# Kernel tuning notes

Measured on AMD Instinct MI355X. Metric: run time of the kernel, lower is better.

Reference implementation:

```python
import jax, jax.numpy as jnp
import numpy as np

B, SQ, SK, H, NH = 2, 2048, 2048, 2048, 16
HD = H // NH  # 128
NEG = -1e9


def setup_inputs() -> dict:
    key = jax.random.key(0)
    ks = jax.random.split(key, 8)
    hidden_states = jax.random.normal(ks[0], (B, SQ, H), dtype=jnp.float32)
    # key already transposed/expanded for baddbmm: [B*nh, head_dim, key_len]
    k = jax.random.normal(ks[1], (B * NH, HD, SK), dtype=jnp.float32)
    v = jax.random.normal(ks[2], (B, NH, SK, HD), dtype=jnp.float32)
    # additive float causal mask [B, 1, Sq, Sk]
    causal = jnp.tril(jnp.ones((SQ, SK), dtype=bool))
    attention_mask = jnp.where(causal, 0.0, NEG).astype(jnp.float32)
    attention_mask = jnp.broadcast_to(attention_mask[None, None], (B, 1, SQ, SK))
    w_q = jax.random.normal(ks[3], (H, H), dtype=jnp.float32) * 0.02
    b_q = jnp.zeros((H,), dtype=jnp.float32)
    w_proj = jax.random.normal(ks[4], (H, H), dtype=jnp.float32) * 0.02
    b_proj = jnp.zeros((H,), dtype=jnp.float32)
    return {
        "hidden_states": hidden_states,
        "key": k,
        "value": v,
        "attention_mask": attention_mask,
        "w_q": w_q,
        "b_q": b_q,
        "w_proj": w_proj,
        "b_proj": b_proj,
    }


def reference(hidden_states, key, value, attention_mask, w_q, b_q, w_proj, b_proj):
    dtype = hidden_states.dtype
    scale = 1.0 / (HD ** 0.5)  # scale_attn_weights=True, attention_multiplier=None
    # q projection: [B, Sq, H] -> [B, nh, Sq, hd]
    q = hidden_states @ w_q.T + b_q
    q = q.reshape(B, SQ, NH, HD).transpose(0, 2, 1, 3)
    # key comes in as [B*nh, hd, Sk]
    k = key.reshape(B, NH, HD, SK)
    # scores = mask + scale * q @ k  (baddbmm with beta=1)
    scores = attention_mask + scale * jnp.einsum("bhqd,bhdk->bhqk", q, k)
    # softmax in fp32 (attention_softmax_in_fp32=True), cast back
    probs = jax.nn.softmax(scores.astype(jnp.float32), axis=-1).astype(dtype)
    # attn_pdrop=0 -> no dropout
    out = jnp.einsum("bhqk,bhkd->bhqd", probs, value)  # [B, nh, Sq, hd]
    out = out.transpose(0, 2, 1, 3).reshape(B, SQ, H)
    out = out @ w_proj.T + b_proj  # resid_pdrop=0 -> no dropout
    return out
```

## Files before the change

### kernel.cpp

```cpp
#include <hip/hip_runtime.h>
#include <hip/hip_bf16.h>

typedef __bf16 bf16;
typedef __bf16 bf16x4 __attribute__((ext_vector_type(4)));
typedef __bf16 bf16x8 __attribute__((ext_vector_type(8)));
typedef float  f32x4  __attribute__((ext_vector_type(4)));
typedef float  f32x16 __attribute__((ext_vector_type(16)));
typedef unsigned int u32;

#define B_   2
#define SQ_  2048
#define SK_  2048
#define H_   2048
#define NH_  16
#define HD_  128
#define BH_  (B_*NH_)

__device__ inline void gl_lds16(const bf16* g, bf16* l) {
  __builtin_amdgcn_global_load_lds(
      (const __attribute__((address_space(1))) u32*)(const void*)g,
      (__attribute__((address_space(3))) u32*)(void*)l,
      16, 0, 0);
}

__device__ inline float exp2_fast(float x) {
  float r; asm("v_exp_f32 %0, %1" : "=v"(r) : "v"(x)); return r;
}

union PW { u32 w[4]; bf16x8 v; };

__global__ __launch_bounds__(256) void cvt3_f32_bf16(const float* __restrict__ a, bf16* __restrict__ ao,
                                                     const float* __restrict__ b, bf16* __restrict__ bo,
                                                     const float* __restrict__ c, bf16* __restrict__ co) {
  const int blk = blockIdx.x;
  const float* in; bf16* out; int n4, bstart, nblk;
  if (blk < 1024)      { in = a; out = ao; n4 = (B_ * SQ_ * H_) / 4; bstart = 0;    nblk = 1024; }
  else if (blk < 1536) { in = b; out = bo; n4 = (H_ * H_) / 4;       bstart = 1024; nblk = 512; }
  else                 { in = c; out = co; n4 = (H_ * H_) / 4;       bstart = 1536; nblk = 512; }
  int i = (blk - bstart) * 256 + threadIdx.x;
  const int stride = nblk * 256;
  for (; i < n4; i += stride) {
    float4 v = ((const float4*)in)[i];
    bf16x4 w; w[0] = (bf16)v.x; w[1] = (bf16)v.y; w[2] = (bf16)v.z; w[3] = (bf16)v.w;
    ((bf16x4*)out)[i] = w;
  }
}

__global__ __launch_bounds__(256) void transpose_cvt2(const float* __restrict__ key,
                                                      const float* __restrict__ value,
                                                      bf16* __restrict__ kout,
                                                      bf16* __restrict__ vout) {
  __shared__ float tile[64][65];
  const int id = blockIdx.x;
  const float* src; bf16* dst; int R, C, r0, c0, bh;
  if (id < 2048) {
    src = key; dst = kout; R = HD_; C = SK_;
    c0 = (id & 31) * 64; r0 = ((id >> 5) & 1) * 64; bh = id >> 6;
  } else {
    const int j = id - 2048;
    src = value; dst = vout; R = SK_; C = HD_;
    c0 = (j & 1) * 64; r0 = ((j >> 1) & 31) * 64; bh = j >> 6;
  }
  src += (size_t)bh * R * C;
  dst += (size_t)bh * R * C;
  const int t = threadIdx.x;
  const int tx = t & 15, ty = t >> 4;
#pragma unroll
  for (int p = 0; p < 4; ++p) {
    int rr = ty + p * 16;
    float4 v = *(const float4*)&src[(size_t)(r0 + rr) * C + c0 + tx * 4];
    tile[rr][tx * 4 + 0] = v.x; tile[rr][tx * 4 + 1] = v.y;
    tile[rr][tx * 4 + 2] = v.z; tile[rr][tx * 4 + 3] = v.w;
  }
  __syncthreads();
#pragma unroll
  for (int p = 0; p < 4; ++p) {
    int cc = ty + p * 16;
    bf16x4 w;
#pragma unroll
    for (int i = 0; i < 4; ++i) w[i] = (bf16)tile[tx * 4 + i][cc];
    *(bf16x4*)&dst[(size_t)(c0 + cc) * R + r0 + tx * 4] = w;
  }
}

template <typename OutT>
__global__ __launch_bounds__(256) void gemm_bt(const bf16* __restrict__ A,
                                               const bf16* __restrict__ Bw,
                                               const float* __restrict__ bias,
                                               OutT* __restrict__ C,
                                               int M, int N, int K, float osc) {
  __shared__ bf16 Abuf[128 * 32];
  __shared__ bf16 Bbuf[128 * 32];
  const int nbn = N >> 7;
  int wg = blockIdx.x, nwg = gridDim.x;
  int swz = (nwg & 7) ? wg : ((wg & 7) * (nwg >> 3) + (wg >> 3));
  int bm = swz / nbn, bn = swz % nbn;
  const int t = threadIdx.x, lane = t & 63, wid = t >> 6;
  const int r = lane & 15, g = lane >> 4;
  const int wr = wid >> 1, wc = wid & 1;
  const size_t m0 = (size_t)bm * 128, n0 = (size_t)bn * 128;

  f32x4 acc[4][4];
#pragma unroll
  for (int m = 0; m < 4; ++m)
#pragma unroll
    for (int n = 0; n < 4; ++n) acc[m][n] = (f32x4){0.f, 0.f, 0.f, 0.f};

  for (int k0 = 0; k0 < K; k0 += 32) {
    __syncthreads();
#pragma unroll
    for (int p = 0; p < 2; ++p) {
      int c = p * 256 + t;
      int row = c >> 2, off = c & 3;
      gl_lds16(A + (m0 + row) * K + k0 + off * 8, &Abuf[(p * 256 + wid * 64) * 8]);
      gl_lds16(Bw + (n0 + row) * K + k0 + off * 8, &Bbuf[(p * 256 + wid * 64) * 8]);
    }
    __syncthreads();
    bf16x8 af[4], bfr[4];
#pragma unroll
    for (int m = 0; m < 4; ++m)
      af[m] = *(const bf16x8*)&Abuf[(wr * 64 + m * 16 + r) * 32 + g * 8];
#pragma unroll
    for (int n = 0; n < 4; ++n)
      bfr[n] = *(const bf16x8*)&Bbuf[(wc * 64 + n * 16 + r) * 32 + g * 8];
#pragma unroll
    for (int m = 0; m < 4; ++m)
#pragma unroll
      for (int n = 0; n < 4; ++n)
        acc[m][n] = __builtin_amdgcn_mfma_f32_16x16x32_bf16(af[m], bfr[n], acc[m][n], 0, 0, 0);
  }

  float bv[4];
#pragma unroll
  for (int n = 0; n < 4; ++n) bv[n] = bias[n0 + wc * 64 + n * 16 + r];
#pragma unroll
  for (int m = 0; m < 4; ++m)
#pragma unroll
    for (int n = 0; n < 4; ++n)
#pragma unroll
      for (int rr = 0; rr < 4; ++rr) {
        size_t row = m0 + wr * 64 + m * 16 + g * 4 + rr;
        size_t col = n0 + wc * 64 + n * 16 + r;
        C[row * N + col] = (OutT)((acc[m][n][rr] + bv[n]) * osc);
      }
}

__global__ __launch_bounds__(256, 2) void flash_attn(const bf16* __restrict__ Q,
                                                     const bf16* __restrict__ Kt,
                                                     const bf16* __restrict__ Vt,
                                                     bf16* __restrict__ O,
                                                     bf16* __restrict__ part,
                                                     float2* __restrict__ mlbuf) {
  __shared__ bf16 Klds[2][64 * 128];
  __shared__ bf16 Vlds[2][64 * 128];

  const int id = blockIdx.x;
  const int pr = (id >> 3) & 7;
  const int hf = (id >> 6) & 1;
  const int bh = (id & 7) + 8 * (id >> 7);
  const int qtA = 15 - pr, qtB = pr;
  const int nA = 2 * qtA + 2, nB = 2 * qtB + 2;
  const int b = bh >> 4, h = bh & 15;
  const int t = threadIdx.x, lane = t & 63, wid = t >> 6;
  const int l5 = lane & 31, hiL = lane >> 5;

  const bf16* Kbase = Kt + (size_t)bh * SK_ * HD_;
  const bf16* Vbase = Vt + (size_t)bh * HD_ * SK_;

  u32 kSrc[4], vSrc[4];
#pragma unroll
  for (int p = 0; p < 4; ++p) {
    int c = p * 256 + t;
    { int row = c >> 4, off = c & 15, src = off ^ (row & 15);
      kSrc[p] = (u32)(row * HD_ + src * 8); }
    { int srow = c >> 4, j = c & 15, gj = j ^ (srow & 15);
      int d = srow * 2 + (gj >> 3);
      vSrc[p] = (u32)(d * SK_ + (gj & 7) * 8); }
  }

  int cur = 0;
  const int npass = hf ? 2 : 1;
#pragma unroll 1
  for (int ps = 0; ps < npass; ++ps) {
    int qt, lo, hi, partial;
    if (!hf)          { qt = qtA; lo = 0;  hi = 17; partial = 1; }
    else if (ps == 0) { qt = qtA; lo = 17; hi = nA; partial = 1; }
    else              { qt = qtB; lo = 0;  hi = nB; partial = 0; }
    const int qbw = qt * 128 + wid * 32;
    const int q_lane = qbw + l5;

    bf16x8 qf[8];
    {
      const size_t qrow = (size_t)(b * SQ_ + q_lane) * H_ + (size_t)h * HD_;
#pragma unroll
      for (int dt = 0; dt < 8; ++dt)
        qf[dt] = *(const bf16x8*)&Q[qrow + dt * 16 + 8 * hiL];
    }

    f32x16 acc[4];
#pragma unroll
    for (int n = 0; n < 4; ++n)
#pragma unroll
      for (int e = 0; e < 16; ++e) acc[n][e] = 0.f;
    float mrun = -3.0e38f, lpart = 0.f;

    {
      const size_t ks = (size_t)lo * (64 * HD_), vs = (size_t)lo * 64;
#pragma unroll
      for (int p = 0; p < 4; ++p) {
        gl_lds16(Kbase + ks + kSrc[p], &Klds[cur][(p * 256 + wid * 64) * 8]);
        gl_lds16(Vbase + vs + vSrc[p], &Vlds[cur][(p * 256 + wid * 64) * 8]);
      }
    }
    asm volatile("s_waitcnt vmcnt(0)" ::: "memory");
    __syncthreads();

#pragma unroll 1
    for (int st = lo; st < hi; ++st) {
      if (st + 1 < hi) {
        const size_t ks = (size_t)(st + 1) * (64 * HD_), vs = (size_t)(st + 1) * 64;
#pragma unroll
        for (int p = 0; p < 4; ++p) {
          gl_lds16(Kbase + ks + kSrc[p], &Klds[cur ^ 1][(p * 256 + wid * 64) * 8]);
          gl_lds16(Vbase + vs + vSrc[p], &Vlds[cur ^ 1][(p * 256 + wid * 64) * 8]);
        }
      }
      const int s0 = st * 64;

      if (s0 <= qbw + 31) {
        f32x16 sv0, sv1;
#pragma unroll
        for (int e = 0; e < 16; ++e) { sv0[e] = 0.f; sv1[e] = 0.f; }
        __builtin_amdgcn_s_setprio(1);
#pragma unroll
        for (int dt = 0; dt < 8; ++dt) {
          const int dch = ((2 * dt + hiL) ^ (l5 & 15)) * 8;
          bf16x8 kf0 = *(const bf16x8*)&Klds[cur][l5 * 128 + dch];
          bf16x8 kf1 = *(const bf16x8*)&Klds[cur][(32 + l5) * 128 + dch];
          sv0 = __builtin_amdgcn_mfma_f32_32x32x16_bf16(kf0, qf[dt], sv0, 0, 0, 0);
          sv1 = __builtin_amdgcn_mfma_f32_32x32x16_bf16(kf1, qf[dt], sv1, 0, 0, 0);
        }
        __builtin_amdgcn_s_setprio(0);

        if (s0 + 63 > qbw) {
#pragma unroll
          for (int r2 = 0; r2 < 16; ++r2) {
            const int kl = (r2 & 3) + 8 * (r2 >> 2) + 4 * hiL;
            if (s0 + kl > q_lane)      sv0[r2] = -3.0e38f;
            if (s0 + 32 + kl > q_lane) sv1[r2] = -3.0e38f;
          }
        }

        float pm = -3.0e38f;
#pragma unroll
        for (int r2 = 0; r2 < 16; ++r2) pm = fmaxf(pm, fmaxf(sv0[r2], sv1[r2]));
        pm = fmaxf(pm, __shfl_xor(pm, 32));
        if (!__all(pm <= mrun + 10.0f ? 1 : 0)) {
          const float mnew = fmaxf(mrun, pm);
          const float corr = exp2_fast(mrun - mnew);
          mrun = mnew; lpart *= corr;
          const int cb = __float_as_int(corr);
#pragma unroll
          for (int r2 = 0; r2 < 16; ++r2) {
            const int q2 = (r2 & 3) + 8 * (r2 >> 2) + 4 * hiL;
            const float cc = __int_as_float(__builtin_amdgcn_ds_bpermute(q2 * 4, cb));
#pragma unroll
            for (int n = 0; n < 4; ++n) acc[n][r2] *= cc;
          }
        }

        float psum = 0.f;
#pragma unroll
        for (int r2 = 0; r2 < 16; ++r2) {
          sv0[r2] = exp2_fast(sv0[r2] - mrun); psum += sv0[r2];
          sv1[r2] = exp2_fast(sv1[r2] - mrun); psum += sv1[r2];
        }
        lpart += psum;

        bf16x8 pa[4];
#pragma unroll
        for (int h2 = 0; h2 < 2; ++h2) {
          u32 pk[8], px[8];
#pragma unroll
          for (int j = 0; j < 8; ++j) {
            union { bf16 hh[2]; u32 u; } tt;
            float plo = h2 ? sv1[2 * j] : sv0[2 * j];
            float phi = h2 ? sv1[2 * j + 1] : sv0[2 * j + 1];
            tt.hh[0] = (bf16)plo; tt.hh[1] = (bf16)phi;
            pk[j] = tt.u;
          }
#pragma unroll
          for (int j = 0; j < 8; ++j) px[j] = (u32)__shfl_xor((int)pk[j], 32);
          PW a0, a1;
          a0.w[0] = hiL ? px[2] : pk[0]; a0.w[1] = hiL ? px[3] : pk[1];
          a0.w[2] = hiL ? pk[2] : px[0]; a0.w[3] = hiL ? pk[3] : px[1];
          a1.w[0] = hiL ? px[6] : pk[4]; a1.w[1] = hiL ? px[7] : pk[5];
          a1.w[2] = hiL ? pk[6] : px[4]; a1.w[3] = hiL ? pk[7] : px[5];
          pa[2 * h2]     = a0.v;
          pa[2 * h2 + 1] = a1.v;
        }

        __builtin_amdgcn_s_setprio(1);
#pragma unroll
        for (int n = 0; n < 4; ++n) {
          const int sr = n * 16 + (l5 >> 1);
#pragma unroll
          for (int kt = 0; kt < 4; ++kt) {
            const int jj = ((((l5 & 1) << 3) | (2 * kt + hiL)) ^ (l5 >> 1));
            bf16x8 vf = *(const bf16x8*)&Vlds[cur][sr * 128 + jj * 8];
            acc[n] = __builtin_amdgcn_mfma_f32_32x32x16_bf16(pa[kt], vf, acc[n], 0, 0, 0);
          }
        }
        __builtin_amdgcn_s_setprio(0);
      }

      asm volatile("s_waitcnt vmcnt(0)" ::: "memory");
      __syncthreads();
      cur ^= 1;
    }

    float ltot = lpart + __shfl_xor(lpart, 32);
    if (partial) {
      const int slot = (hf * 8 + pr) * 32 + bh;
      bf16* pbase = part + (size_t)slot * (128 * 128);
#pragma unroll
      for (int n = 0; n < 4; ++n)
#pragma unroll
        for (int r2 = 0; r2 < 16; ++r2) {
          const int rowt = wid * 32 + (r2 & 3) + 8 * (r2 >> 2) + 4 * hiL;
          pbase[rowt * 128 + n * 32 + l5] = (bf16)acc[n][r2];
        }
      if (lane < 32)
        mlbuf[(size_t)slot * 128 + wid * 32 + lane] = float2{mrun, ltot};
    } else {
      const float inv = 1.0f / ltot;
      const int ib = __float_as_int(inv);
#pragma unroll
      for (int r2 = 0; r2 < 16; ++r2) {
        const int q2 = (r2 & 3) + 8 * (r2 >> 2) + 4 * hiL;
        const float ic = __int_as_float(__builtin_amdgcn_ds_bpermute(q2 * 4, ib));
        const size_t rowg = (size_t)(b * SQ_ + qbw + q2);
#pragma unroll
        for (int n = 0; n < 4; ++n)
          O[rowg * H_ + (size_t)h * HD_ + n * 32 + l5] = (bf16)(acc[n][r2] * ic);
      }
    }
  }
}

__global__ __launch_bounds__(256) void flash_merge(const bf16* __restrict__ part,
                                                   const float2* __restrict__ mlbuf,
                                                   bf16* __restrict__ O) {
  const int gid = blockIdx.x * 256 + threadIdx.x;
  const int idx = gid >> 4;
  const int d8 = (gid & 15) * 8;
  const int row = idx & 127;
  const int bh = (idx >> 7) & 31;
  const int pr = idx >> 12;
  const int qtA = 15 - pr;
  const int b = bh >> 4, h = bh & 15;
  const int slot0 = pr * 32 + bh;
  const int slot1 = (8 + pr) * 32 + bh;
  const float2 ml0 = mlbuf[(size_t)slot0 * 128 + row];
  const float2 ml1 = mlbuf[(size_t)slot1 * 128 + row];
  const float M = fmaxf(ml0.x, ml1.x);
  const float c0 = exp2_fast(ml0.x - M);
  const float c1 = exp2_fast(ml1.x - M);
  const float inv = 1.0f / (c0 * ml0.y + c1 * ml1.y);
  const bf16x8 a0 = *(const bf16x8*)&part[(size_t)slot0 * (128 * 128) + row * 128 + d8];
  const bf16x8 a1 = *(const bf16x8*)&part[(size_t)slot1 * (128 * 128) + row * 128 + d8];
  bf16x8 o;
#pragma unroll
  for (int j = 0; j < 8; ++j)
    o[j] = (bf16)((c0 * (float)a0[j] + c1 * (float)a1[j]) * inv);
  const size_t orow = (size_t)(b * SQ_ + qtA * 128 + row);
  *(bf16x8*)&O[orow * H_ + (size_t)h * HD_ + d8] = o;
}

extern "C" void kernel_launch(void* const* d_in, const int* in_sizes, int n_in,
                              void* d_out, int out_size, void* d_ws, size_t ws_size,
                              hipStream_t stream) {
  const float* hidden = (const float*)d_in[0];
  const float* key    = (const float*)d_in[1];
  const float* value  = (const float*)d_in[2];
  const float* w_q    = (const float*)d_in[4];
  const float* b_q    = (const float*)d_in[5];
  const float* w_proj = (const float*)d_in[6];
  const float* b_proj = (const float*)d_in[7];
  float* out = (float*)d_out;

  const size_t N_HID = (size_t)B_ * SQ_ * H_;
  const size_t N_W   = (size_t)H_ * H_;
  const size_t N_KV  = (size_t)BH_ * SK_ * HD_;
  const float SC2 = 0.08838834764831845f * 1.4426950408889634f;

  bf16* hid_bf  = (bf16*)d_ws;
  bf16* wq_bf   = hid_bf + N_HID;
  bf16* wp_bf   = wq_bf + N_W;
  bf16* k_bf    = wp_bf + N_W;
  bf16* vt_bf   = k_bf + N_KV;
  bf16* q_bf    = vt_bf + N_KV;
  bf16* part_bf = q_bf + N_HID;
  float2* ml_bf = (float2*)(part_bf + (size_t)512 * 128 * 128);
  bf16* attn_bf = hid_bf;

  cvt3_f32_bf16<<<2048, 256, 0, stream>>>(hidden, hid_bf, w_q, wq_bf, w_proj, wp_bf);
  transpose_cvt2<<<4096, 256, 0, stream>>>(key, value, k_bf, vt_bf);

  gemm_bt<bf16><<<(B_ * SQ_ / 128) * (H_ / 128), 256, 0, stream>>>(
      hid_bf, wq_bf, b_q, q_bf, B_ * SQ_, H_, H_, SC2);

  flash_attn<<<512, 256, 0, stream>>>(q_bf, k_bf, vt_bf, attn_bf, part_bf, ml_bf);
  flash_merge<<<2048, 256, 0, stream>>>(part_bf, ml_bf, attn_bf);

  gemm_bt<float><<<(B_ * SQ_ / 128) * (H_ / 128), 256, 0, stream>>>(
      attn_bf, wp_bf, b_proj, out, B_ * SQ_, H_, H_, 1.0f);
}
```

Measured before the change: 211.1 us.

## Defer P·V MFMAs by one tile to overlap with next QK and softmax

The P·V product for tile i is now issued in iteration i+1, right after the QK^T MFMAs for that tile and before its softmax. The aim is to let matrix work overlap the exp/max/shuffle work of softmax within a wave. V gets a third LDS buffer so the previous tile's V stays resident while the next one loads. A final drain step after the loop handles the last pending tile. The cost is a larger LDS footprint (V grows from two to three buffers), more live registers for the held P fragments, and an extra barrier at the start of each pass.

```diff
diff --git a/kernel.cpp b/kernel.cpp
--- a/kernel.cpp
+++ b/kernel.cpp
@@ -152,7 +152,7 @@
                                                      bf16* __restrict__ part,
                                                      float2* __restrict__ mlbuf) {
   __shared__ bf16 Klds[2][64 * 128];
-  __shared__ bf16 Vlds[2][64 * 128];
+  __shared__ bf16 Vlds[3][64 * 128];
 
   const int id = blockIdx.x;
   const int pr = (id >> 3) & 7;
@@ -178,7 +178,6 @@
       vSrc[p] = (u32)(d * SK_ + (gj & 7) * 8); }
   }
 
-  int cur = 0;
   const int npass = hf ? 2 : 1;
 #pragma unroll 1
   for (int ps = 0; ps < npass; ++ps) {
@@ -204,12 +203,17 @@
       for (int e = 0; e < 16; ++e) acc[n][e] = 0.f;
     float mrun = -3.0e38f, lpart = 0.f;
 
+    bf16x8 paP[4];
+    bool have_prev = false;
+    int kc = 0, vp = 2, vc = 0, vn = 1;
+
+    __syncthreads();
     {
       const size_t ks = (size_t)lo * (64 * HD_), vs = (size_t)lo * 64;
 #pragma unroll
       for (int p = 0; p < 4; ++p) {
-        gl_lds16(Kbase + ks + kSrc[p], &Klds[cur][(p * 256 + wid * 64) * 8]);
-        gl_lds16(Vbase + vs + vSrc[p], &Vlds[cur][(p * 256 + wid * 64) * 8]);
+        gl_lds16(Kbase + ks + kSrc[p], &Klds[0][(p * 256 + wid * 64) * 8]);
+        gl_lds16(Vbase + vs + vSrc[p], &Vlds[0][(p * 256 + wid * 64) * 8]);
       }
     }
     asm volatile("s_waitcnt vmcnt(0)" ::: "memory");
@@ -221,27 +225,47 @@
         const size_t ks = (size_t)(st + 1) * (64 * HD_), vs = (size_t)(st + 1) * 64;
 #pragma unroll
         for (int p = 0; p < 4; ++p) {
-          gl_lds16(Kbase + ks + kSrc[p], &Klds[cur ^ 1][(p * 256 + wid * 64) * 8]);
-          gl_lds16(Vbase + vs + vSrc[p], &Vlds[cur ^ 1][(p * 256 + wid * 64) * 8]);
+          gl_lds16(Kbase + ks + kSrc[p], &Klds[kc ^ 1][(p * 256 + wid * 64) * 8]);
+          gl_lds16(Vbase + vs + vSrc[p], &Vlds[vn][(p * 256 + wid * 64) * 8]);
         }
       }
       const int s0 = st * 64;
-
-      if (s0 <= qbw + 31) {
-        f32x16 sv0, sv1;
+      const bool act = (s0 <= qbw + 31);
+
+      f32x16 sv0, sv1;
+      if (act) {
 #pragma unroll
         for (int e = 0; e < 16; ++e) { sv0[e] = 0.f; sv1[e] = 0.f; }
         __builtin_amdgcn_s_setprio(1);
 #pragma unroll
         for (int dt = 0; dt < 8; ++dt) {
           const int dch = ((2 * dt + hiL) ^ (l5 & 15)) * 8;
-          bf16x8 kf0 = *(const bf16x8*)&Klds[cur][l5 * 128 + dch];
-          bf16x8 kf1 = *(const bf16x8*)&Klds[cur][(32 + l5) * 128 + dch];
+          bf16x8 kf0 = *(const bf16x8*)&Klds[kc][l5 * 128 + dch];
+          bf16x8 kf1 = *(const bf16x8*)&Klds[kc][(32 + l5) * 128 + dch];
           sv0 = __builtin_amdgcn_mfma_f32_32x32x16_bf16(kf0, qf[dt], sv0, 0, 0, 0);
           sv1 = __builtin_amdgcn_mfma_f32_32x32x16_bf16(kf1, qf[dt], sv1, 0, 0, 0);
         }
         __builtin_amdgcn_s_setprio(0);
-
+      }
+
+      if (have_prev) {
+        const bf16* vbuf = &Vlds[vp][0];
+        __builtin_amdgcn_s_setprio(1);
+#pragma unroll
+        for (int n = 0; n < 4; ++n) {
+          const int sr = n * 16 + (l5 >> 1);
+#pragma unroll
+          for (int kt = 0; kt < 4; ++kt) {
+            const int jj = ((((l5 & 1) << 3) | (2 * kt + hiL)) ^ (l5 >> 1));
+            bf16x8 vf = *(const bf16x8*)&vbuf[sr * 128 + jj * 8];
+            acc[n] = __builtin_amdgcn_mfma_f32_32x32x16_bf16(paP[kt], vf, acc[n], 0, 0, 0);
+          }
+        }
+        __builtin_amdgcn_s_setprio(0);
+        have_prev = false;
+      }
+
+      if (act) {
         if (s0 + 63 > qbw) {
 #pragma unroll
           for (int r2 = 0; r2 < 16; ++r2) {
@@ -277,7 +301,6 @@
         }
         lpart += psum;
 
-        bf16x8 pa[4];
 #pragma unroll
         for (int h2 = 0; h2 < 2; ++h2) {
           u32 pk[8], px[8];
@@ -296,27 +319,31 @@
           a0.w[2] = hiL ? pk[2] : px[0]; a0.w[3] = hiL ? pk[3] : px[1];
           a1.w[0] = hiL ? px[6] : pk[4]; a1.w[1] = hiL ? px[7] : pk[5];
           a1.w[2] = hiL ? pk[6] : px[4]; a1.w[3] = hiL ? pk[7] : px[5];
-          pa[2 * h2]     = a0.v;
-          pa[2 * h2 + 1] = a1.v;
-        }
-
-        __builtin_amdgcn_s_setprio(1);
-#pragma unroll
-        for (int n = 0; n < 4; ++n) {
-          const int sr = n * 16 + (l5 >> 1);
-#pragma unroll
-          for (int kt = 0; kt < 4; ++kt) {
-            const int jj = ((((l5 & 1) << 3) | (2 * kt + hiL)) ^ (l5 >> 1));
-            bf16x8 vf = *(const bf16x8*)&Vlds[cur][sr * 128 + jj * 8];
-            acc[n] = __builtin_amdgcn_mfma_f32_32x32x16_bf16(pa[kt], vf, acc[n], 0, 0, 0);
-          }
-        }
-        __builtin_amdgcn_s_setprio(0);
+          paP[2 * h2]     = a0.v;
+          paP[2 * h2 + 1] = a1.v;
+        }
+        have_prev = true;
       }
 
       asm volatile("s_waitcnt vmcnt(0)" ::: "memory");
       __syncthreads();
-      cur ^= 1;
+      kc ^= 1;
+      const int ovp = vp; vp = vc; vc = vn; vn = ovp;
+    }
+
+    if (have_prev) {
+      const bf16* vbuf = &Vlds[vp][0];
+#pragma unroll
+      for (int n = 0; n < 4; ++n) {
+        const int sr = n * 16 + (l5 >> 1);
+#pragma unroll
+        for (int kt = 0; kt < 4; ++kt) {
+          const int jj = ((((l5 & 1) << 3) | (2 * kt + hiL)) ^ (l5 >> 1));
+          bf16x8 vf = *(const bf16x8*)&vbuf[sr * 128 + jj * 8];
+          acc[n] = __builtin_amdgcn_mfma_f32_32x32x16_bf16(paP[kt], vf, acc[n], 0, 0, 0);
+        }
+      }
+      have_prev = false;
     }
 
     float ltot = lpart + __shfl_xor(lpart, 32);
```

After: 211.3 us. Within noise of the previous version (+0.1%).
